# Optimization experiments

Measured on AMD Instinct MI355X. Metric: run time of the kernel, lower is better.

Reference implementation:

```python
import jax, jax.numpy as jnp
import numpy as np

HEADS = 16
HIDDEN = 1024
DH = HIDDEN // HEADS
STD = 0.02


def setup_inputs() -> dict:
    key = jax.random.key(0)
    ks = jax.random.split(key, 12)
    B, S = 4, 2048
    inp = {
        'q': jax.random.normal(ks[0], (B, S, HIDDEN), jnp.float32),
        'k': jax.random.normal(ks[1], (B, S, HIDDEN), jnp.float32),
        'v': jax.random.normal(ks[2], (B, S, HIDDEN), jnp.float32),
        'mask': jax.random.randint(ks[3], (B, S), 0, 2, jnp.int32),
        # linear layers: weight [out,in] torch-style, init N(0, 0.02), bias 0
        'wq': STD * jax.random.normal(ks[4], (HIDDEN, HIDDEN), jnp.float32),
        'bq': jnp.zeros((HIDDEN,), jnp.float32),
        'wk': STD * jax.random.normal(ks[5], (HIDDEN, HIDDEN), jnp.float32),
        'bk': jnp.zeros((HIDDEN,), jnp.float32),
        'wv': STD * jax.random.normal(ks[6], (HIDDEN, HIDDEN), jnp.float32),
        'bv': jnp.zeros((HIDDEN,), jnp.float32),
        'wo': STD * jax.random.normal(ks[7], (HIDDEN, HIDDEN), jnp.float32),
        'bo': jnp.zeros((HIDDEN,), jnp.float32),
    }
    return inp


def _split_heads(x):
    B, S, _ = x.shape
    return x.reshape(B, S, HEADS, DH).transpose(0, 2, 1, 3)  # [B,H,S,dh]


def reference(q, k, v, mask, wq, bq, wk, bk, wv, bv, wo, bo):
    B, S, _ = q.shape
    qh = _split_heads(q @ wq.T + bq)
    kh = _split_heads(k @ wk.T + bk)
    vh = _split_heads(v @ wv.T + bv)
    scale = 1.0 / jnp.sqrt(jnp.float32(DH))
    corr = jnp.einsum('bhqd,bhkd->bhqk', qh, kh) * scale  # [B,H,S,S]
    # original masks QUERY rows: mask [B,S] -> [B,1,S,1] broadcast over heads & keys
    row_mask = (mask != 0)[:, None, :, None]
    corr = jnp.where(row_mask, corr, jnp.float32(-1e9))
    prob = jax.nn.softmax(corr, axis=-1)
    # dropout p=0.0 (eval / deterministic reference)
    hidden = jnp.einsum('bhqk,bhkd->bhqd', prob, vh)
    hidden = hidden.transpose(0, 2, 1, 3).reshape(B, S, HIDDEN)
    return hidden @ wo.T + bo
```

## Files before the change

kernel.cpp:

```cpp
#include <hip/hip_runtime.h>

#define BATCH 4
#define SEQ 2048
#define HEADS 16
#define DHEAD 64
#define HID 1024
#define MROWS (BATCH * SEQ)
#define QSCALE 0.1803368801111092f

typedef unsigned short u16;
typedef unsigned int u32;
typedef __attribute__((ext_vector_type(4))) float f32x4;
typedef __attribute__((ext_vector_type(8))) short bf16x8;

#define MFMA16(a, b, c) __builtin_amdgcn_mfma_f32_16x16x32_bf16((a), (b), (c), 0, 0, 0)
#define EXP2F(x) __builtin_amdgcn_exp2f(x)

__device__ __forceinline__ u16 f2bf(float f) {
  union { float f; u32 i; } x; x.f = f;
  u32 r = x.i + 0x7fffu + ((x.i >> 16) & 1u);
  return (u16)(r >> 16);
}

__device__ __forceinline__ void lds16(const u16* g, u16* s) {
  __builtin_amdgcn_global_load_lds(
      (const __attribute__((address_space(1))) void*)g,
      (__attribute__((address_space(3))) void*)s, 16, 0, 0);
}

__device__ __forceinline__ void stage8f(const float* __restrict__ g, u16* s) {
  const float4 a = *(const float4*)g;
  const float4 b = *(const float4*)(g + 4);
  ushort4 lo, hi;
  lo.x = f2bf(a.x); lo.y = f2bf(a.y); lo.z = f2bf(a.z); lo.w = f2bf(a.w);
  hi.x = f2bf(b.x); hi.y = f2bf(b.y); hi.z = f2bf(b.z); hi.w = f2bf(b.w);
  *(ushort4*)s = lo;
  *(ushort4*)(s + 4) = hi;
}

struct CvtArgs {
  const float* src[7];
  u16* dst[7];
};
__global__ __launch_bounds__(256) void cvt7(CvtArgs args, int yoff, int nact) {
  const int y = blockIdx.y + yoff;
  const int i = (blockIdx.x * 256 + threadIdx.x) * 8;
  if (y < 3) {
    if (i < nact) stage8f(args.src[y] + i, args.dst[y] + i);
  } else {
    if (i < 4 * (1 << 20)) {
      const int j = i >> 20, off = i & ((1 << 20) - 1);
      stage8f(args.src[3 + j] + off, args.dst[3 + j] + off);
    }
  }
}

template<bool ADMA, bool BDMA>
__device__ __forceinline__ void gemm_core(
    const void* __restrict__ Av, const void* __restrict__ Wv,
    int tid, int m0, int n0, u16* As, u16* Bs, f32x4 (&acc)[4][4])
{
  const int srow = tid >> 2, cslot = tid & 3;
  const int gc = cslot ^ ((srow >> 1) & 3);
  const int w = tid >> 6, l = tid & 63;
  const int quad = l >> 4, l15 = l & 15;
  const int sw = (l15 >> 1) & 3;
  const int wm = (w & 1) << 6, wn = (w >> 1) << 6;

  for (int k0 = 0; k0 < HID; k0 += 32) {
    if (ADMA) {
      const u16* ag = (const u16*)Av + (size_t)(m0 + srow) * HID + k0 + gc * 8;
      lds16(ag, &As[tid * 8]);
      lds16(ag + (size_t)64 * HID, &As[2048 + tid * 8]);
    } else {
      const float* ag = (const float*)Av + (size_t)(m0 + srow) * HID + k0 + gc * 8;
      stage8f(ag, &As[srow * 32 + cslot * 8]);
      stage8f(ag + (size_t)64 * HID, &As[(64 + srow) * 32 + cslot * 8]);
    }
    if (BDMA) {
      const u16* bg = (const u16*)Wv + (size_t)(n0 + srow) * HID + k0 + gc * 8;
      lds16(bg, &Bs[tid * 8]);
      lds16(bg + (size_t)64 * HID, &Bs[2048 + tid * 8]);
    } else {
      const float* bg = (const float*)Wv + (size_t)(n0 + srow) * HID + k0 + gc * 8;
      stage8f(bg, &Bs[srow * 32 + cslot * 8]);
      stage8f(bg + (size_t)64 * HID, &Bs[(64 + srow) * 32 + cslot * 8]);
    }
    __syncthreads();

    bf16x8 a[4], b[4];
    #pragma unroll
    for (int i = 0; i < 4; ++i)
      a[i] = *(const bf16x8*)&As[(wm + i * 16 + l15) * 32 + (quad ^ sw) * 8];
    #pragma unroll
    for (int j = 0; j < 4; ++j)
      b[j] = *(const bf16x8*)&Bs[(wn + j * 16 + l15) * 32 + (quad ^ sw) * 8];
    #pragma unroll
    for (int i = 0; i < 4; ++i)
      #pragma unroll
      for (int j = 0; j < 4; ++j)
        acc[i][j] = MFMA16(a[i], b[j], acc[i][j]);
    __syncthreads();
  }
}

template<bool ADMA, bool BDMA>
__global__ __launch_bounds__(256) void gemm_qkv(
    const void* __restrict__ xq, const void* __restrict__ xk,
    const void* __restrict__ xv,
    const void* __restrict__ wqv, const void* __restrict__ wkv,
    const void* __restrict__ wvv,
    const float* __restrict__ bq, const float* __restrict__ bk,
    const float* __restrict__ bv, const int* __restrict__ Mask,
    u16* __restrict__ qh, u16* __restrict__ kh, u16* __restrict__ vt)
{
  __shared__ u16 As[128 * 32];
  __shared__ u16 Bs[128 * 32];
  const int z = blockIdx.z;
  const void* A = (z == 0) ? xq : (z == 1) ? xk : xv;
  const void* W = (z == 0) ? wqv : (z == 1) ? wkv : wvv;
  const float* Bias = (z == 0) ? bq : (z == 1) ? bk : bv;

  const int tid = threadIdx.x;
  const int m0 = blockIdx.x << 7, n0 = blockIdx.y << 7;
  f32x4 acc[4][4] = {};
  gemm_core<ADMA, BDMA>(A, W, tid, m0, n0, As, Bs, acc);

  const int w = tid >> 6, l = tid & 63;
  const int quad = l >> 4, l15 = l & 15;
  const int wm = (w & 1) << 6, wn = (w >> 1) << 6;

  if (z <= 1) {
    u16* Out = (z == 0) ? qh : kh;
    #pragma unroll
    for (int i = 0; i < 4; ++i) {
      float fl[4];
      #pragma unroll
      for (int r = 0; r < 4; ++r) {
        const int m = m0 + wm + i * 16 + (quad << 2) + r;
        fl[r] = (z == 0) ? (Mask[m] ? QSCALE : 0.f) : 1.f;
      }
      #pragma unroll
      for (int j = 0; j < 4; ++j) {
        const int n = n0 + wn + j * 16 + l15;
        const float bias = Bias[n];
        const int h = n >> 6, d = n & 63;
        #pragma unroll
        for (int r = 0; r < 4; ++r) {
          const int m = m0 + wm + i * 16 + (quad << 2) + r;
          const int bb = m >> 11, s = m & (SEQ - 1);
          Out[((size_t)(bb * HEADS + h) * SEQ + s) * DHEAD + d] =
              f2bf((acc[i][j][r] + bias) * fl[r]);
        }
      }
    }
  } else {
    const int sblk = (m0 + wm) & (SEQ - 1);
    const int bb = (m0 + wm) >> 11;
    #pragma unroll
    for (int j = 0; j < 4; ++j) {
      const int n = n0 + wn + j * 16 + l15;
      const float bias = Bias[n];
      const int h = n >> 6, d = n & 63;
      u16* base = vt + ((size_t)(bb * HEADS + h) * DHEAD + d) * SEQ + sblk;
      #pragma unroll
      for (int r = 0; r < 4; ++r) {
        ushort4 pk;
        pk.x = f2bf(acc[0][j][r] + bias);
        pk.y = f2bf(acc[1][j][r] + bias);
        pk.z = f2bf(acc[2][j][r] + bias);
        pk.w = f2bf(acc[3][j][r] + bias);
        *(ushort4*)(base + ((quad << 2) + r) * 4) = pk;
      }
    }
  }
}

template<bool BDMA>
__global__ __launch_bounds__(256) void gemm_out(
    const u16* __restrict__ hidden, const void* __restrict__ wov,
    const float* __restrict__ bo, float* __restrict__ Out)
{
  __shared__ u16 As[128 * 32];
  __shared__ u16 Bs[128 * 32];
  const int tid = threadIdx.x;
  const int m0 = blockIdx.x << 7, n0 = blockIdx.y << 7;
  f32x4 acc[4][4] = {};
  gemm_core<true, BDMA>(hidden, wov, tid, m0, n0, As, Bs, acc);

  const int w = tid >> 6, l = tid & 63;
  const int quad = l >> 4, l15 = l & 15;
  const int wm = (w & 1) << 6, wn = (w >> 1) << 6;
  #pragma unroll
  for (int j = 0; j < 4; ++j) {
    const int n = n0 + wn + j * 16 + l15;
    const float bias = bo[n];
    #pragma unroll
    for (int i = 0; i < 4; ++i) {
      const int mb = m0 + wm + i * 16 + (quad << 2);
      #pragma unroll
      for (int r = 0; r < 4; ++r)
        Out[(size_t)(mb + r) * HID + n] = acc[i][j][r] + bias;
    }
  }
}

__global__ __launch_bounds__(128, 2) void attn_mfma(
    const u16* __restrict__ QH, const u16* __restrict__ KH,
    const u16* __restrict__ VT, u16* __restrict__ Hidden)
{
  __shared__ u16 QP[128 * 64];
  __shared__ u16 Ks[2][64 * 32];
  __shared__ u16 Vt[2][64 * 32];

  const int tid = threadIdx.x;
  const int w = tid >> 6, l = tid & 63;
  const int quad = l >> 4, l15 = l & 15;
  const int sw = (l15 >> 1) & 3;
  const int srow = tid >> 2, cslot = tid & 3;
  const int gc = cslot ^ ((srow >> 1) & 3);

  const int lin = blockIdx.y * 16 + blockIdx.x;
  const int bh = lin & 63, b = bh >> 4, h = bh & 15;
  const int q0 = (lin >> 6) << 7;

  const u16* qbase = QH + (size_t)bh * SEQ * DHEAD;
  const u16* kbase = KH + (size_t)bh * SEQ * DHEAD;
  const u16* vbase = VT + (size_t)bh * DHEAD * SEQ;

  #pragma unroll
  for (int hh = 0; hh < 2; ++hh)
    #pragma unroll
    for (int part = 0; part < 4; ++part)
      lds16(qbase + (size_t)(q0 + part * 32 + srow) * DHEAD + hh * 32 + gc * 8,
            &QP[hh * 4096 + part * 1024 + tid * 8]);
  __syncthreads();

  bf16x8 aq[2][4];
  #pragma unroll
  for (int hh = 0; hh < 2; ++hh)
    #pragma unroll
    for (int i = 0; i < 4; ++i)
      aq[hh][i] = *(const bf16x8*)
          &QP[hh * 4096 + (w * 64 + i * 16 + l15) * 32 + (quad ^ sw) * 8];

  float lsum[4][4] = {};
  f32x4 o[4][4] = {};

  for (int t0 = 0; t0 < SEQ; t0 += 64) {
    __syncthreads();
    #pragma unroll
    for (int hh = 0; hh < 2; ++hh)
      #pragma unroll
      for (int part = 0; part < 2; ++part) {
        lds16(kbase + (size_t)(t0 + part * 32 + srow) * DHEAD + hh * 32 + gc * 8,
              &Ks[hh][part * 1024 + tid * 8]);
        lds16(vbase + (size_t)(part * 32 + srow) * SEQ + t0 + hh * 32 + gc * 8,
              &Vt[hh][part * 1024 + tid * 8]);
      }
    __syncthreads();

    f32x4 s[4][4] = {};
    #pragma unroll
    for (int j = 0; j < 4; ++j)
      #pragma unroll
      for (int hh = 0; hh < 2; ++hh) {
        const bf16x8 bk = *(const bf16x8*)
            &Ks[hh][(j * 16 + l15) * 32 + (quad ^ sw) * 8];
        #pragma unroll
        for (int i = 0; i < 4; ++i)
          s[i][j] = MFMA16(aq[hh][i], bk, s[i][j]);
      }

    #pragma unroll
    for (int i = 0; i < 4; ++i)
      #pragma unroll
      for (int r = 0; r < 4; ++r) {
        const float p0 = EXP2F(s[i][0][r]);
        const float p1 = EXP2F(s[i][1][r]);
        const float p2 = EXP2F(s[i][2][r]);
        const float p3 = EXP2F(s[i][3][r]);
        lsum[i][r] += (p0 + p1) + (p2 + p3);
        const int row = w * 64 + i * 16 + (quad << 2) + r;
        const int cs = ((l15 >> 1) ^ (row & 7)) * 8 + (l15 & 1) * 4;
        ushort4 pk;
        pk.x = f2bf(p0); pk.y = f2bf(p1); pk.z = f2bf(p2); pk.w = f2bf(p3);
        *(ushort4*)&QP[row * 64 + cs] = pk;
      }

    #pragma unroll
    for (int hh = 0; hh < 2; ++hh) {
      bf16x8 ap[4];
      #pragma unroll
      for (int i = 0; i < 4; ++i) {
        const int row = w * 64 + i * 16 + l15;
        ap[i] = *(const bf16x8*)
            &QP[row * 64 + (((hh * 4 + quad) ^ (row & 7)) << 3)];
      }
      #pragma unroll
      for (int j = 0; j < 4; ++j) {
        const bf16x8 vb = *(const bf16x8*)
            &Vt[hh][(j * 16 + l15) * 32 + (quad ^ sw) * 8];
        #pragma unroll
        for (int i = 0; i < 4; ++i)
          o[i][j] = MFMA16(ap[i], vb, o[i][j]);
      }
    }
  }

  float inv[4][4];
  #pragma unroll
  for (int i = 0; i < 4; ++i)
    #pragma unroll
    for (int r = 0; r < 4; ++r) {
      float t = lsum[i][r];
      #pragma unroll
      for (int off = 1; off < 16; off <<= 1)
        t += __shfl_xor(t, off);
      inv[i][r] = 1.f / t;
    }

  #pragma unroll
  for (int i = 0; i < 4; ++i)
    #pragma unroll
    for (int j = 0; j < 4; ++j)
      #pragma unroll
      for (int r = 0; r < 4; ++r) {
        const int qrow = q0 + w * 64 + i * 16 + (quad << 2) + r;
        Hidden[((size_t)(b * SEQ + qrow)) * HID + h * DHEAD + j * 16 + l15] =
            f2bf(o[i][j][r] * inv[i][r]);
      }
}

extern "C" void kernel_launch(void* const* d_in, const int* in_sizes, int n_in,
                              void* d_out, int out_size, void* d_ws, size_t ws_size,
                              hipStream_t stream) {
  const float* q  = (const float*)d_in[0];
  const float* k  = (const float*)d_in[1];
  const float* v  = (const float*)d_in[2];
  const int* mask = (const int*)d_in[3];
  const float* wq = (const float*)d_in[4];
  const float* bq = (const float*)d_in[5];
  const float* wk = (const float*)d_in[6];
  const float* bk = (const float*)d_in[7];
  const float* wv = (const float*)d_in[8];
  const float* bv = (const float*)d_in[9];
  const float* wo = (const float*)d_in[10];
  const float* bo = (const float*)d_in[11];

  const size_t SEG = (size_t)MROWS * HID;
  const size_t WSEG = (size_t)HID * HID;
  const dim3 gq(MROWS / 128, HID / 128, 3);
  const dim3 go(MROWS / 128, HID / 128);
  const dim3 ga(SEQ / 128, BATCH * HEADS);

  const size_t planFULL = (6 * SEG + 4 * WSEG) * sizeof(u16);
  const size_t planMID  = (4 * SEG + 4 * WSEG) * sizeof(u16);

  if (ws_size >= planFULL) {
    u16* qb  = (u16*)d_ws;
    u16* kb  = qb + SEG;
    u16* vb  = kb + SEG;
    u16* qh  = vb + SEG;
    u16* kh  = qh + SEG;
    u16* vt  = kh + SEG;
    u16* wqb = vt + SEG;
    u16* wkb = wqb + WSEG;
    u16* wvb = wkb + WSEG;
    u16* wob = wvb + WSEG;
    u16* hidden = qb;

    CvtArgs ca;
    ca.src[0] = q;  ca.dst[0] = qb;
    ca.src[1] = k;  ca.dst[1] = kb;
    ca.src[2] = v;  ca.dst[2] = vb;
    ca.src[3] = wq; ca.dst[3] = wqb;
    ca.src[4] = wk; ca.dst[4] = wkb;
    ca.src[5] = wv; ca.dst[5] = wvb;
    ca.src[6] = wo; ca.dst[6] = wob;
    cvt7<<<dim3(SEG / 2048, 4), 256, 0, stream>>>(ca, 0, (int)SEG);

    gemm_qkv<true, true><<<gq, 256, 0, stream>>>(qb, kb, vb, wqb, wkb, wvb,
                                                 bq, bk, bv, mask, qh, kh, vt);
    attn_mfma<<<ga, 128, 0, stream>>>(qh, kh, vt, hidden);
    gemm_out<true><<<go, 256, 0, stream>>>(hidden, wob, bo, (float*)d_out);
  } else if (ws_size >= planMID) {
    u16* wqb = (u16*)d_ws;
    u16* wkb = wqb + WSEG;
    u16* wvb = wkb + WSEG;
    u16* wob = wvb + WSEG;
    u16* qh = wob + WSEG;
    u16* kh = qh + SEG;
    u16* vt = kh + SEG;
    u16* hidden = vt + SEG;

    CvtArgs ca;
    ca.src[0] = ca.src[1] = ca.src[2] = q;
    ca.dst[0] = ca.dst[1] = ca.dst[2] = wqb;
    ca.src[3] = wq; ca.dst[3] = wqb;
    ca.src[4] = wk; ca.dst[4] = wkb;
    ca.src[5] = wv; ca.dst[5] = wvb;
    ca.src[6] = wo; ca.dst[6] = wob;
    cvt7<<<dim3(4 * WSEG / 2048, 1), 256, 0, stream>>>(ca, 3, 0);

    gemm_qkv<false, true><<<gq, 256, 0, stream>>>(q, k, v, wqb, wkb, wvb,
                                                  bq, bk, bv, mask, qh, kh, vt);
    attn_mfma<<<ga, 128, 0, stream>>>(qh, kh, vt, hidden);
    gemm_out<true><<<go, 256, 0, stream>>>(hidden, wob, bo, (float*)d_out);
  } else {
    u16* qh = (u16*)d_ws;
    u16* kh = qh + SEG;
    u16* vt = kh + SEG;
    u16* hidden = vt + SEG;

    gemm_qkv<false, false><<<gq, 256, 0, stream>>>(q, k, v, wq, wk, wv,
                                                   bq, bk, bv, mask, qh, kh, vt);
    attn_mfma<<<ga, 128, 0, stream>>>(qh, kh, vt, hidden);
    gemm_out<false><<<go, 256, 0, stream>>>(hidden, wo, bo, (float*)d_out);
  }
}
```

Measured before the change: 358.9 us.

## Split attention over key halves with combine kernel and larger 256-thread blocks

The attention kernel now uses 256-thread blocks covering 256 query rows, and can optionally split the key range into two halves across separate blocks. Each half writes unnormalized partial outputs and row sums, and a new combine kernel adds them and normalizes. The aim is more blocks per head for better CU occupancy and more K/V reuse per load, at the cost of extra workspace traffic and an extra launch. The bf16 packing of P is also simplified to truncation, and the row sum is taken from the truncated values.

After: 545.7 us. 1.52x slower.

```diff
diff --git a/kernel.cpp b/kernel.cpp
--- a/kernel.cpp
+++ b/kernel.cpp
@@ -16,11 +16,15 @@
 #define MFMA16(a, b, c) __builtin_amdgcn_mfma_f32_16x16x32_bf16((a), (b), (c), 0, 0, 0)
 #define EXP2F(x) __builtin_amdgcn_exp2f(x)
 
+__device__ __forceinline__ float bflo(u32 w) { union { u32 i; float f; } x; x.i = w << 16; return x.f; }
+__device__ __forceinline__ float bfhi(u32 w) { union { u32 i; float f; } x; x.i = w & 0xffff0000u; return x.f; }
 __device__ __forceinline__ u16 f2bf(float f) {
   union { float f; u32 i; } x; x.f = f;
   u32 r = x.i + 0x7fffu + ((x.i >> 16) & 1u);
   return (u16)(r >> 16);
 }
+__device__ __forceinline__ u32 fbits(float f) { union { float f; u32 i; } x; x.f = f; return x.i; }
+__device__ __forceinline__ float asf(u32 i) { union { u32 i; float f; } x; x.i = i; return x.f; }
 
 __device__ __forceinline__ void lds16(const u16* g, u16* s) {
   __builtin_amdgcn_global_load_lds(
@@ -205,11 +209,13 @@
   }
 }
 
-__global__ __launch_bounds__(128, 2) void attn_mfma(
+template<int MODE>
+__global__ __launch_bounds__(256, 3) void attn_mfma(
     const u16* __restrict__ QH, const u16* __restrict__ KH,
-    const u16* __restrict__ VT, u16* __restrict__ Hidden)
+    const u16* __restrict__ VT, u16* __restrict__ Hidden,
+    void* __restrict__ OPart, float* __restrict__ LSum)
 {
-  __shared__ u16 QP[128 * 64];
+  __shared__ u16 QP[256 * 64];
   __shared__ u16 Ks[2][64 * 32];
   __shared__ u16 Vt[2][64 * 32];
 
@@ -220,9 +226,13 @@
   const int srow = tid >> 2, cslot = tid & 3;
   const int gc = cslot ^ ((srow >> 1) & 3);
 
-  const int lin = blockIdx.y * 16 + blockIdx.x;
+  const int lin = blockIdx.x;
   const int bh = lin & 63, b = bh >> 4, h = bh & 15;
-  const int q0 = (lin >> 6) << 7;
+  const int qt = (lin >> 6) & 7;
+  const int z  = (MODE == 0) ? 0 : (lin >> 9);
+  const int q0 = qt << 8;
+  const int nk = (MODE == 0) ? SEQ : SEQ / 2;
+  const int tb = z * (SEQ / 2);
 
   const u16* qbase = QH + (size_t)bh * SEQ * DHEAD;
   const u16* kbase = KH + (size_t)bh * SEQ * DHEAD;
@@ -232,8 +242,8 @@
   for (int hh = 0; hh < 2; ++hh)
     #pragma unroll
     for (int part = 0; part < 4; ++part)
-      lds16(qbase + (size_t)(q0 + part * 32 + srow) * DHEAD + hh * 32 + gc * 8,
-            &QP[hh * 4096 + part * 1024 + tid * 8]);
+      lds16(qbase + (size_t)(q0 + part * 64 + srow) * DHEAD + hh * 32 + gc * 8,
+            &QP[hh * 8192 + part * 2048 + tid * 8]);
   __syncthreads();
 
   bf16x8 aq[2][4];
@@ -242,22 +252,19 @@
     #pragma unroll
     for (int i = 0; i < 4; ++i)
       aq[hh][i] = *(const bf16x8*)
-          &QP[hh * 4096 + (w * 64 + i * 16 + l15) * 32 + (quad ^ sw) * 8];
+          &QP[hh * 8192 + (w * 64 + i * 16 + l15) * 32 + (quad ^ sw) * 8];
 
   float lsum[4][4] = {};
   f32x4 o[4][4] = {};
 
-  for (int t0 = 0; t0 < SEQ; t0 += 64) {
+  for (int t = 0; t < nk; t += 64) {
+    const int t0 = tb + t;
     __syncthreads();
     #pragma unroll
-    for (int hh = 0; hh < 2; ++hh)
-      #pragma unroll
-      for (int part = 0; part < 2; ++part) {
-        lds16(kbase + (size_t)(t0 + part * 32 + srow) * DHEAD + hh * 32 + gc * 8,
-              &Ks[hh][part * 1024 + tid * 8]);
-        lds16(vbase + (size_t)(part * 32 + srow) * SEQ + t0 + hh * 32 + gc * 8,
-              &Vt[hh][part * 1024 + tid * 8]);
-      }
+    for (int hh = 0; hh < 2; ++hh) {
+      lds16(kbase + (size_t)(t0 + srow) * DHEAD + hh * 32 + gc * 8, &Ks[hh][tid * 8]);
+      lds16(vbase + (size_t)srow * SEQ + t0 + hh * 32 + gc * 8, &Vt[hh][tid * 8]);
+    }
     __syncthreads();
 
     f32x4 s[4][4] = {};
@@ -276,27 +283,27 @@
     for (int i = 0; i < 4; ++i)
       #pragma unroll
       for (int r = 0; r < 4; ++r) {
-        const float p0 = EXP2F(s[i][0][r]);
-        const float p1 = EXP2F(s[i][1][r]);
-        const float p2 = EXP2F(s[i][2][r]);
-        const float p3 = EXP2F(s[i][3][r]);
-        lsum[i][r] += (p0 + p1) + (p2 + p3);
-        const int row = w * 64 + i * 16 + (quad << 2) + r;
+        const u32 u0 = fbits(EXP2F(s[i][0][r]));
+        const u32 u1 = fbits(EXP2F(s[i][1][r]));
+        const u32 u2 = fbits(EXP2F(s[i][2][r]));
+        const u32 u3 = fbits(EXP2F(s[i][3][r]));
+        lsum[i][r] += (asf(u0 & 0xffff0000u) + asf(u1 & 0xffff0000u)) +
+                      (asf(u2 & 0xffff0000u) + asf(u3 & 0xffff0000u));
+        const u32 lo = (u0 >> 16) | (u1 & 0xffff0000u);
+        const u32 hi = (u2 >> 16) | (u3 & 0xffff0000u);
+        const int row = i * 16 + (quad << 2) + r;
         const int cs = ((l15 >> 1) ^ (row & 7)) * 8 + (l15 & 1) * 4;
-        ushort4 pk;
-        pk.x = f2bf(p0); pk.y = f2bf(p1); pk.z = f2bf(p2); pk.w = f2bf(p3);
-        *(ushort4*)&QP[row * 64 + cs] = pk;
+        uint2 pk; pk.x = lo; pk.y = hi;
+        *(uint2*)&QP[w * 4096 + row * 64 + cs] = pk;
       }
 
     #pragma unroll
     for (int hh = 0; hh < 2; ++hh) {
       bf16x8 ap[4];
       #pragma unroll
-      for (int i = 0; i < 4; ++i) {
-        const int row = w * 64 + i * 16 + l15;
+      for (int i = 0; i < 4; ++i)
         ap[i] = *(const bf16x8*)
-            &QP[row * 64 + (((hh * 4 + quad) ^ (row & 7)) << 3)];
-      }
+            &QP[w * 4096 + (i * 16 + l15) * 64 + (((hh * 4 + quad) ^ (l15 & 7)) << 3)];
       #pragma unroll
       for (int j = 0; j < 4; ++j) {
         const bf16x8 vb = *(const bf16x8*)
@@ -308,7 +315,6 @@
     }
   }
 
-  float inv[4][4];
   #pragma unroll
   for (int i = 0; i < 4; ++i)
     #pragma unroll
@@ -317,19 +323,81 @@
       #pragma unroll
       for (int off = 1; off < 16; off <<= 1)
         t += __shfl_xor(t, off);
-      inv[i][r] = 1.f / t;
-    }
-
-  #pragma unroll
-  for (int i = 0; i < 4; ++i)
-    #pragma unroll
-    for (int j = 0; j < 4; ++j)
-      #pragma unroll
-      for (int r = 0; r < 4; ++r) {
-        const int qrow = q0 + w * 64 + i * 16 + (quad << 2) + r;
-        Hidden[((size_t)(b * SEQ + qrow)) * HID + h * DHEAD + j * 16 + l15] =
-            f2bf(o[i][j][r] * inv[i][r]);
-      }
+      lsum[i][r] = t;
+    }
+
+  if (MODE == 0) {
+    #pragma unroll
+    for (int i = 0; i < 4; ++i)
+      #pragma unroll
+      for (int j = 0; j < 4; ++j)
+        #pragma unroll
+        for (int r = 0; r < 4; ++r) {
+          const int qrow = q0 + w * 64 + i * 16 + (quad << 2) + r;
+          Hidden[((size_t)(b * SEQ + qrow)) * HID + h * DHEAD + j * 16 + l15] =
+              f2bf(o[i][j][r] / lsum[i][r]);
+        }
+  } else {
+    const size_t obase = (size_t)z * (SEQ * (size_t)64 * DHEAD)
+                       + (size_t)bh * SEQ * DHEAD;
+    #pragma unroll
+    for (int i = 0; i < 4; ++i)
+      #pragma unroll
+      for (int j = 0; j < 4; ++j)
+        #pragma unroll
+        for (int r = 0; r < 4; ++r) {
+          const int s0 = q0 + w * 64 + i * 16 + (quad << 2) + r;
+          const size_t idx = obase + (size_t)s0 * DHEAD + j * 16 + l15;
+          if (MODE == 2) ((float*)OPart)[idx] = o[i][j][r];
+          else           ((u16*)OPart)[idx]   = f2bf(o[i][j][r]);
+        }
+    if (l15 == 0) {
+      #pragma unroll
+      for (int i = 0; i < 4; ++i)
+        #pragma unroll
+        for (int r = 0; r < 4; ++r) {
+          const int s0 = q0 + w * 64 + i * 16 + (quad << 2) + r;
+          LSum[z * (64 * SEQ) + bh * SEQ + s0] = lsum[i][r];
+        }
+    }
+  }
+}
+
+template<int MODE>
+__global__ __launch_bounds__(256) void combine(
+    const void* __restrict__ OPart, const float* __restrict__ LSum,
+    u16* __restrict__ Hidden)
+{
+  const int g = (blockIdx.x * 256 + threadIdx.x) * 8;
+  const int d = g & 63;
+  const int rest = g >> 6;
+  const int bh = rest >> 11, s = rest & (SEQ - 1);
+  const int b = bh >> 4, h = bh & 15;
+  const float inv = 1.f / (LSum[rest] + LSum[64 * SEQ + rest]);
+  const size_t half = (size_t)64 * SEQ * DHEAD;
+
+  float v[8];
+  if (MODE == 2) {
+    const float* o = (const float*)OPart;
+    #pragma unroll
+    for (int t = 0; t < 8; ++t) v[t] = o[g + t] + o[half + g + t];
+  } else {
+    const u16* o = (const u16*)OPart;
+    const uint4 a = *(const uint4*)(o + g);
+    const uint4 c = *(const uint4*)(o + half + g);
+    v[0] = bflo(a.x) + bflo(c.x); v[1] = bfhi(a.x) + bfhi(c.x);
+    v[2] = bflo(a.y) + bflo(c.y); v[3] = bfhi(a.y) + bfhi(c.y);
+    v[4] = bflo(a.z) + bflo(c.z); v[5] = bfhi(a.z) + bfhi(c.z);
+    v[6] = bflo(a.w) + bflo(c.w); v[7] = bfhi(a.w) + bfhi(c.w);
+  }
+  ushort4 p0, p1;
+  p0.x = f2bf(v[0] * inv); p0.y = f2bf(v[1] * inv);
+  p0.z = f2bf(v[2] * inv); p0.w = f2bf(v[3] * inv);
+  p1.x = f2bf(v[4] * inv); p1.y = f2bf(v[5] * inv);
+  p1.z = f2bf(v[6] * inv); p1.w = f2bf(v[7] * inv);
+  u16* out = Hidden + ((size_t)(b * SEQ + s)) * HID + h * DHEAD + d;
+  *(ushort4*)out = p0;
+  *(ushort4*)(out + 4) = p1;
 }
 
 extern "C" void kernel_launch(void* const* d_in, const int* in_sizes, int n_in,
@@ -352,12 +420,13 @@
   const size_t WSEG = (size_t)HID * HID;
   const dim3 gq(MROWS / 128, HID / 128, 3);
   const dim3 go(MROWS / 128, HID / 128);
-  const dim3 ga(SEQ / 128, BATCH * HEADS);
-
-  const size_t planFULL = (6 * SEG + 4 * WSEG) * sizeof(u16);
-  const size_t planMID  = (4 * SEG + 4 * WSEG) * sizeof(u16);
-
-  if (ws_size >= planFULL) {
+
+  const size_t FULLB    = (6 * SEG + 4 * WSEG) * sizeof(u16);
+  const size_t LSUMB    = 2 * 64 * SEQ * sizeof(float);
+  const size_t SPLIT32B = FULLB + 2 * SEG * sizeof(float) + LSUMB;
+  const size_t SPLIT16B = FULLB + 2 * SEG * sizeof(u16) + LSUMB;
+
+  if (ws_size >= FULLB) {
     u16* qb  = (u16*)d_ws;
     u16* kb  = qb + SEG;
     u16* vb  = kb + SEG;
@@ -369,6 +438,9 @@
     u16* wvb = wkb + WSEG;
     u16* wob = wvb + WSEG;
     u16* hidden = qb;
+    void* opart = (void*)(wob + WSEG);
+    float* lsum32 = (float*)((char*)opart +
+        ((ws_size >= SPLIT32B) ? 2 * SEG * sizeof(float) : 2 * SEG * sizeof(u16)));
 
     CvtArgs ca;
     ca.src[0] = q;  ca.dst[0] = qb;
@@ -382,40 +454,50 @@
 
     gemm_qkv<true, true><<<gq, 256, 0, stream>>>(qb, kb, vb, wqb, wkb, wvb,
                                                  bq, bk, bv, mask, qh, kh, vt);
-    attn_mfma<<<ga, 128, 0, stream>>>(qh, kh, vt, hidden);
-    gemm_out<true><<<go, 256, 0, stream>>>(hidden, wob, bo, (float*)d_out);
-  } else if (ws_size >= planMID) {
-    u16* wqb = (u16*)d_ws;
-    u16* wkb = wqb + WSEG;
-    u16* wvb = wkb + WSEG;
-    u16* wob = wvb + WSEG;
-    u16* qh = wob + WSEG;
-    u16* kh = qh + SEG;
-    u16* vt = kh + SEG;
-    u16* hidden = vt + SEG;
-
-    CvtArgs ca;
-    ca.src[0] = ca.src[1] = ca.src[2] = q;
-    ca.dst[0] = ca.dst[1] = ca.dst[2] = wqb;
-    ca.src[3] = wq; ca.dst[3] = wqb;
-    ca.src[4] = wk; ca.dst[4] = wkb;
-    ca.src[5] = wv; ca.dst[5] = wvb;
-    ca.src[6] = wo; ca.dst[6] = wob;
-    cvt7<<<dim3(4 * WSEG / 2048, 1), 256, 0, stream>>>(ca, 3, 0);
-
-    gemm_qkv<false, true><<<gq, 256, 0, stream>>>(q, k, v, wqb, wkb, wvb,
-                                                  bq, bk, bv, mask, qh, kh, vt);
-    attn_mfma<<<ga, 128, 0, stream>>>(qh, kh, vt, hidden);
+    if (ws_size >= SPLIT32B) {
+      attn_mfma<2><<<1024, 256, 0, stream>>>(qh, kh, vt, hidden, opart, lsum32);
+      combine<2><<<SEG / 2048, 256, 0, stream>>>(opart, lsum32, hidden);
+    } else if (ws_size >= SPLIT16B) {
+      attn_mfma<1><<<1024, 256, 0, stream>>>(qh, kh, vt, hidden, opart, lsum32);
+      combine<1><<<SEG / 2048, 256, 0, stream>>>(opart, lsum32, hidden);
+    } else {
+      attn_mfma<0><<<512, 256, 0, stream>>>(qh, kh, vt, hidden, nullptr, nullptr);
+    }
     gemm_out<true><<<go, 256, 0, stream>>>(hidden, wob, bo, (float*)d_out);
   } else {
-    u16* qh = (u16*)d_ws;
-    u16* kh = qh + SEG;
-    u16* vt = kh + SEG;
-    u16* hidden = vt + SEG;
-
-    gemm_qkv<false, false><<<gq, 256, 0, stream>>>(q, k, v, wq, wk, wv,
-                                                   bq, bk, bv, mask, qh, kh, vt);
-    attn_mfma<<<ga, 128, 0, stream>>>(qh, kh, vt, hidden);
-    gemm_out<false><<<go, 256, 0, stream>>>(hidden, wo, bo, (float*)d_out);
-  }
-}
+    const size_t MIDB = (4 * SEG + 4 * WSEG) * sizeof(u16);
+    if (ws_size >= MIDB) {
+      u16* wqb = (u16*)d_ws;
+      u16* wkb = wqb + WSEG;
+      u16* wvb = wkb + WSEG;
+      u16* wob = wvb + WSEG;
+      u16* qh = wob + WSEG;
+      u16* kh = qh + SEG;
+      u16* vt = kh + SEG;
+      u16* hidden = vt + SEG;
+
+      CvtArgs ca;
+      ca.src[0] = ca.src[1] = ca.src[2] = q;
+      ca.dst[0] = ca.dst[1] = ca.dst[2] = wqb;
+      ca.src[3] = wq; ca.dst[3] = wqb;
+      ca.src[4] = wk; ca.dst[4] = wkb;
+      ca.src[5] = wv; ca.dst[5] = wvb;
+      ca.src[6] = wo; ca.dst[6] = wob;
+      cvt7<<<dim3(4 * WSEG / 2048, 1), 256, 0, stream>>>(ca, 3, 0);
+
+      gemm_qkv<false, true><<<gq, 256, 0, stream>>>(q, k, v, wqb, wkb, wvb,
+                                                    bq, bk, bv, mask, qh, kh, vt);
+      attn_mfma<0><<<512, 256, 0, stream>>>(qh, kh, vt, hidden, nullptr, nullptr);
+      gemm_out<true><<<go, 256, 0, stream>>>(hidden, wob, bo, (float*)d_out);
+    } else {
+      u16* qh = (u16*)d_ws;
+      u16* kh = qh + SEG;
+      u16* vt = kh + SEG;
+      u16* hidden = vt + SEG;
+      gemm_qkv<false, false><<<gq, 256, 0, stream>>>(q, k, v, wq, wk, wv,
+                                                     bq, bk, bv, mask, qh, kh, vt);
+      attn_mfma<0><<<512, 256, 0, stream>>>(qh, kh, vt, hidden, nullptr, nullptr);
+      gemm_out<false><<<go, 256, 0, stream>>>(hidden, wo, bo, (float*)d_out);
+    }
+  }
+}
```
